# Performance work log

Hardware: AMD Instinct MI355X
Metric: run time of the kernel (lower is better)

## Reference

```python
import jax, jax.numpy as jnp
import numpy as np

N = 50000
E = 800000
IN_C = 256
OUT_C = 128
HID = 2 * OUT_C  # 256


def setup_inputs() -> dict:
    key = jax.random.key(0)
    ks = jax.random.split(key, 8)
    def glorot(k, fan_in, fan_out):
        lim = (6.0 / (fan_in + fan_out)) ** 0.5
        return jax.random.uniform(k, (fan_in, fan_out), jnp.float32, -lim, lim)
    x = jax.random.normal(ks[0], (N, IN_C), dtype=jnp.float32)
    edge_index = jax.random.randint(ks[1], (2, E), 0, N, dtype=jnp.int64)
    return {
        "x": x,
        "edge_index": edge_index,
        "W1": glorot(ks[2], IN_C, HID),
        "b1": jnp.zeros((HID,), jnp.float32),
        "W_mu": glorot(ks[3], HID, OUT_C),
        "b_mu": jnp.zeros((OUT_C,), jnp.float32),
        "W_ls": glorot(ks[4], HID, OUT_C),
        "b_ls": jnp.zeros((OUT_C,), jnp.float32),
    }


def _gcn_norm(edge_index, n):
    # PyG GCNConv default: add self-loops, symmetric normalization D^-1/2 A D^-1/2
    loop = jnp.arange(n, dtype=edge_index.dtype)
    src = jnp.concatenate([edge_index[0], loop])  # [E+N]
    dst = jnp.concatenate([edge_index[1], loop])
    deg = jax.ops.segment_sum(jnp.ones_like(dst, dtype=jnp.float32), dst, num_segments=n)
    dinv = jnp.where(deg > 0, jax.lax.rsqrt(deg), 0.0)
    norm = dinv[src] * dinv[dst]  # [E+N]
    return src, dst, norm


def _gcn_conv(x, W, b, src, dst, norm, n):
    h = x @ W                                   # [N, F_out] transform first (F_out < F_in ok)
    msg = h[src] * norm[:, None]                # [E+N, F_out] gather + scale
    out = jax.ops.segment_sum(msg, dst, num_segments=n)  # scatter-add aggregate
    return out + b


def reference(x, edge_index, W1, b1, W_mu, b_mu, W_ls, b_ls):
    n = x.shape[0]
    src, dst, norm = _gcn_norm(edge_index, n)
    h = jax.nn.relu(_gcn_conv(x, W1, b1, src, dst, norm, n))
    mu = _gcn_conv(h, W_mu, b_mu, src, dst, norm, n)
    logstd = _gcn_conv(h, W_ls, b_ls, src, dst, norm, n)
    return (mu, logstd)
```

## Files before the change

### kernel.cpp

```cpp
#include <hip/hip_runtime.h>

#define NN 50000
#define EE 800000
#define NB_FILL 3125
#define NB_PA 12500
#define NB_PB 512

typedef _Float16 half8 __attribute__((ext_vector_type(8)));
typedef float f32x4 __attribute__((ext_vector_type(4)));

__device__ __forceinline__ unsigned short f2h(float f){
  _Float16 h = (_Float16)f; unsigned short u; __builtin_memcpy(&u, &h, 2); return u;
}
__device__ __forceinline__ float h2f(unsigned short u){
  _Float16 h; __builtin_memcpy(&h, &u, 2); return (float)h;
}
__device__ __forceinline__ void split2h(float v, unsigned short* p){
  _Float16 hi = (_Float16)v;
  _Float16 lo = (_Float16)(v - (float)hi);
  __builtin_memcpy(p, &hi, 2);
  __builtin_memcpy(p+1, &lo, 2);
}
__device__ __forceinline__ void gl2lds16(const unsigned short* g, unsigned short* l){
  __builtin_amdgcn_global_load_lds(
    (const __attribute__((address_space(1))) unsigned int*)g,
    (__attribute__((address_space(3))) unsigned int*)l, 16, 0, 0);
}

__device__ __forceinline__ int detect_m(const int* eidx, int* sh){
  int t = threadIdx.x;
  if (t < 64){
    int v = eidx[2*t + 1];
    unsigned long long nz = __ballot(v != 0);
    if (t == 0) *sh = (nz == 0ULL) ? 1 : 0;
  }
  __syncthreads();
  return *sh;
}

__global__ __launch_bounds__(256) void k_prep(const int* __restrict__ eidx,
    const float* __restrict__ X, const float* __restrict__ W1,
    const float* __restrict__ Wmu, const float* __restrict__ Wls,
    int* __restrict__ cnt, int* __restrict__ bk,
    unsigned short* __restrict__ Asp, unsigned short* __restrict__ Bt1,
    unsigned short* __restrict__ Bt2){
  int b = blockIdx.x;
  if (b < NB_FILL){
    __shared__ int msh;
    int m = detect_m(eidx, &msh);
    int e = b*256 + threadIdx.x;
    int sv = m ? eidx[2*e]        : eidx[e];
    int d  = m ? eidx[2*(EE + e)] : eidx[EE + e];
    int p = atomicAdd(&cnt[d], 1);
    if (p < 64) bk[((size_t)d << 6) + p] = sv;
  } else if (b < NB_FILL + NB_PA){
    int gid = (b - NB_FILL)*256 + threadIdx.x;
    int r = gid >> 6, t = gid & 63;
    float4 v = *(const float4*)(X + (size_t)r*256 + t*4);
    __attribute__((aligned(16))) unsigned short sh[8];
    split2h(v.x, sh); split2h(v.y, sh+2); split2h(v.z, sh+4); split2h(v.w, sh+6);
    *(uint4*)(Asp + (size_t)r*512 + t*8) = *(const uint4*)(sh);
  } else {
    int gid = (b - NB_FILL - NB_PA)*256 + threadIdx.x;
    int idx = gid & 65535;
    int n = idx & 255, k = idx >> 8;
    if (gid < 65536){
      unsigned short hq = f2h(W1[k*256 + n]);
      unsigned short* p = Bt1 + (size_t)n*512 + 2*k;
      p[0] = hq; p[1] = hq;
    } else {
      float w = (n < 128) ? Wmu[k*128 + n] : Wls[k*128 + (n - 128)];
      Bt2[(size_t)n*256 + k] = f2h(w);
    }
  }
}

template<int KT, int SCALE>
__global__ __launch_bounds__(256) void k_gemm(const unsigned short* __restrict__ Asp,
                                              const unsigned short* __restrict__ Bt,
                                              unsigned short* __restrict__ C, int M,
                                              const int* __restrict__ cnt){
  __shared__ __align__(16) unsigned short sA[128*64];
  __shared__ __align__(16) unsigned short sB[128*64];
  const int tid  = threadIdx.x;
  const int wave = tid >> 6, lane = tid & 63;
  const int wm = wave >> 1, wn = wave & 1;
  const int quad = lane >> 4, l16 = lane & 15;
  const int tM = blockIdx.x, tN = blockIdx.y;
  const int rsub = lane >> 3;
  const int chs  = (lane & 7) ^ rsub;

  f32x4 acc[4][4] = {};

  for (int kt = 0; kt < KT; ++kt){
    #pragma unroll
    for (int j = 0; j < 4; ++j){
      int q = wave*4 + j;
      int r = q*8 + rsub;
      int arow = tM*128 + r; if (arow >= M) arow = M-1;
      gl2lds16(Asp + (size_t)arow*(KT*64) + kt*64 + chs*8, &sA[q*512]);
      gl2lds16(Bt  + (size_t)(tN*128 + r)*(KT*64) + kt*64 + chs*8, &sB[q*512]);
    }
    __syncthreads();
    #pragma unroll
    for (int ks = 0; ks < 2; ++ks){
      half8 af[4], bfr[4];
      #pragma unroll
      for (int t = 0; t < 4; ++t){
        int R = wm*64 + t*16 + l16;
        af[t]  = *(const half8*)(&sA[R*64 + ((ks*4 + quad) ^ (R & 7))*8]);
      }
      #pragma unroll
      for (int t = 0; t < 4; ++t){
        int R = wn*64 + t*16 + l16;
        bfr[t] = *(const half8*)(&sB[R*64 + ((ks*4 + quad) ^ (R & 7))*8]);
      }
      #pragma unroll
      for (int mt = 0; mt < 4; ++mt)
        #pragma unroll
        for (int nt = 0; nt < 4; ++nt)
          acc[mt][nt] = __builtin_amdgcn_mfma_f32_16x16x32_f16(af[mt], bfr[nt], acc[mt][nt], 0, 0, 0);
    }
    __syncthreads();
  }

  #pragma unroll
  for (int mt = 0; mt < 4; ++mt){
    #pragma unroll
    for (int r = 0; r < 4; ++r){
      int row = tM*128 + wm*64 + mt*16 + quad*4 + r;
      if (row < M){
        float sc = 1.f;
        if (SCALE) sc = rsqrtf((float)(cnt[row] + 1));
        #pragma unroll
        for (int nt = 0; nt < 4; ++nt){
          int cc = tN*128 + wn*64 + nt*16 + l16;
          C[(size_t)row*256 + cc] = f2h(acc[mt][nt][r] * sc);
        }
      }
    }
  }
}

__global__ __launch_bounds__(256) void k_agg_relu(const unsigned short* __restrict__ feat,
    const int* __restrict__ cnt, const int* __restrict__ bkall,
    const float* __restrict__ b1, unsigned short* __restrict__ h1){
  int i = blockIdx.x*4 + (threadIdx.x >> 6);
  int lane = threadIdx.x & 63;
  int f0 = lane*4;
  int deg = cnt[i]; if (deg > 64) deg = 64;
  float di = rsqrtf((float)(deg + 1));
  const int* bk = bkall + ((size_t)i << 6);
  ushort4 hv = *(const ushort4*)(feat + (size_t)i*256 + f0);
  float p0 = h2f(hv.x), p1 = h2f(hv.y), p2 = h2f(hv.z), p3 = h2f(hv.w);
  float q0=0.f,q1=0.f,q2=0.f,q3=0.f, r0=0.f,r1=0.f,r2=0.f,r3=0.f, t0=0.f,t1=0.f,t2=0.f,t3=0.f;
  int e = 0;
  for (; e + 8 <= deg; e += 8){
    int4 sa = *(const int4*)(bk + e);
    int4 sb = *(const int4*)(bk + e + 4);
    ushort4 v0 = *(const ushort4*)(feat + (size_t)sa.x*256 + f0);
    ushort4 v1 = *(const ushort4*)(feat + (size_t)sa.y*256 + f0);
    ushort4 v2 = *(const ushort4*)(feat + (size_t)sa.z*256 + f0);
    ushort4 v3 = *(const ushort4*)(feat + (size_t)sa.w*256 + f0);
    ushort4 v4 = *(const ushort4*)(feat + (size_t)sb.x*256 + f0);
    ushort4 v5 = *(const ushort4*)(feat + (size_t)sb.y*256 + f0);
    ushort4 v6 = *(const ushort4*)(feat + (size_t)sb.z*256 + f0);
    ushort4 v7 = *(const ushort4*)(feat + (size_t)sb.w*256 + f0);
    p0 += h2f(v0.x); p1 += h2f(v0.y); p2 += h2f(v0.z); p3 += h2f(v0.w);
    q0 += h2f(v1.x); q1 += h2f(v1.y); q2 += h2f(v1.z); q3 += h2f(v1.w);
    r0 += h2f(v2.x); r1 += h2f(v2.y); r2 += h2f(v2.z); r3 += h2f(v2.w);
    t0 += h2f(v3.x); t1 += h2f(v3.y); t2 += h2f(v3.z); t3 += h2f(v3.w);
    p0 += h2f(v4.x); p1 += h2f(v4.y); p2 += h2f(v4.z); p3 += h2f(v4.w);
    q0 += h2f(v5.x); q1 += h2f(v5.y); q2 += h2f(v5.z); q3 += h2f(v5.w);
    r0 += h2f(v6.x); r1 += h2f(v6.y); r2 += h2f(v6.z); r3 += h2f(v6.w);
    t0 += h2f(v7.x); t1 += h2f(v7.y); t2 += h2f(v7.z); t3 += h2f(v7.w);
  }
  if (e + 4 <= deg){
    int4 sa = *(const int4*)(bk + e);
    ushort4 v0 = *(const ushort4*)(feat + (size_t)sa.x*256 + f0);
    ushort4 v1 = *(const ushort4*)(feat + (size_t)sa.y*256 + f0);
    ushort4 v2 = *(const ushort4*)(feat + (size_t)sa.z*256 + f0);
    ushort4 v3 = *(const ushort4*)(feat + (size_t)sa.w*256 + f0);
    p0 += h2f(v0.x); p1 += h2f(v0.y); p2 += h2f(v0.z); p3 += h2f(v0.w);
    q0 += h2f(v1.x); q1 += h2f(v1.y); q2 += h2f(v1.z); q3 += h2f(v1.w);
    r0 += h2f(v2.x); r1 += h2f(v2.y); r2 += h2f(v2.z); r3 += h2f(v2.w);
    t0 += h2f(v3.x); t1 += h2f(v3.y); t2 += h2f(v3.z); t3 += h2f(v3.w);
    e += 4;
  }
  for (; e < deg; ++e){
    int s = bk[e];
    ushort4 v = *(const ushort4*)(feat + (size_t)s*256 + f0);
    p0 += h2f(v.x); p1 += h2f(v.y); p2 += h2f(v.z); p3 += h2f(v.w);
  }
  float s0 = p0+q0+r0+t0, s1 = p1+q1+r1+t1, s2 = p2+q2+r2+t2, s3 = p3+q3+r3+t3;
  float4 bb = *(const float4*)(b1 + f0);
  float u0 = fmaxf(di*s0 + bb.x, 0.f);
  float u1 = fmaxf(di*s1 + bb.y, 0.f);
  float u2 = fmaxf(di*s2 + bb.z, 0.f);
  float u3 = fmaxf(di*s3 + bb.w, 0.f);
  ushort4 o;
  o.x = f2h(di*u0); o.y = f2h(di*u1); o.z = f2h(di*u2); o.w = f2h(di*u3);
  *(ushort4*)(h1 + (size_t)i*256 + f0) = o;
}

__global__ __launch_bounds__(256) void k_agg_out(const unsigned short* __restrict__ feat,
    const int* __restrict__ cnt, const int* __restrict__ bkall,
    const float* __restrict__ bmu, const float* __restrict__ bls, float* __restrict__ outp){
  int i = blockIdx.x*4 + (threadIdx.x >> 6);
  int lane = threadIdx.x & 63;
  int f0 = lane*4;
  int deg = cnt[i]; if (deg > 64) deg = 64;
  float di = rsqrtf((float)(deg + 1));
  const int* bk = bkall + ((size_t)i << 6);
  ushort4 hv = *(const ushort4*)(feat + (size_t)i*256 + f0);
  float p0 = h2f(hv.x), p1 = h2f(hv.y), p2 = h2f(hv.z), p3 = h2f(hv.w);
  float q0=0.f,q1=0.f,q2=0.f,q3=0.f, r0=0.f,r1=0.f,r2=0.f,r3=0.f, t0=0.f,t1=0.f,t2=0.f,t3=0.f;
  int e = 0;
  for (; e + 8 <= deg; e += 8){
    int4 sa = *(const int4*)(bk + e);
    int4 sb = *(const int4*)(bk + e + 4);
    ushort4 v0 = *(const ushort4*)(feat + (size_t)sa.x*256 + f0);
    ushort4 v1 = *(const ushort4*)(feat + (size_t)sa.y*256 + f0);
    ushort4 v2 = *(const ushort4*)(feat + (size_t)sa.z*256 + f0);
    ushort4 v3 = *(const ushort4*)(feat + (size_t)sa.w*256 + f0);
    ushort4 v4 = *(const ushort4*)(feat + (size_t)sb.x*256 + f0);
    ushort4 v5 = *(const ushort4*)(feat + (size_t)sb.y*256 + f0);
    ushort4 v6 = *(const ushort4*)(feat + (size_t)sb.z*256 + f0);
    ushort4 v7 = *(const ushort4*)(feat + (size_t)sb.w*256 + f0);
    p0 += h2f(v0.x); p1 += h2f(v0.y); p2 += h2f(v0.z); p3 += h2f(v0.w);
    q0 += h2f(v1.x); q1 += h2f(v1.y); q2 += h2f(v1.z); q3 += h2f(v1.w);
    r0 += h2f(v2.x); r1 += h2f(v2.y); r2 += h2f(v2.z); r3 += h2f(v2.w);
    t0 += h2f(v3.x); t1 += h2f(v3.y); t2 += h2f(v3.z); t3 += h2f(v3.w);
    p0 += h2f(v4.x); p1 += h2f(v4.y); p2 += h2f(v4.z); p3 += h2f(v4.w);
    q0 += h2f(v5.x); q1 += h2f(v5.y); q2 += h2f(v5.z); q3 += h2f(v5.w);
    r0 += h2f(v6.x); r1 += h2f(v6.y); r2 += h2f(v6.z); r3 += h2f(v6.w);
    t0 += h2f(v7.x); t1 += h2f(v7.y); t2 += h2f(v7.z); t3 += h2f(v7.w);
  }
  if (e + 4 <= deg){
    int4 sa = *(const int4*)(bk + e);
    ushort4 v0 = *(const ushort4*)(feat + (size_t)sa.x*256 + f0);
    ushort4 v1 = *(const ushort4*)(feat + (size_t)sa.y*256 + f0);
    ushort4 v2 = *(const ushort4*)(feat + (size_t)sa.z*256 + f0);
    ushort4 v3 = *(const ushort4*)(feat + (size_t)sa.w*256 + f0);
    p0 += h2f(v0.x); p1 += h2f(v0.y); p2 += h2f(v0.z); p3 += h2f(v0.w);
    q0 += h2f(v1.x); q1 += h2f(v1.y); q2 += h2f(v1.z); q3 += h2f(v1.w);
    r0 += h2f(v2.x); r1 += h2f(v2.y); r2 += h2f(v2.z); r3 += h2f(v2.w);
    t0 += h2f(v3.x); t1 += h2f(v3.y); t2 += h2f(v3.z); t3 += h2f(v3.w);
    e += 4;
  }
  for (; e < deg; ++e){
    int s = bk[e];
    ushort4 v = *(const ushort4*)(feat + (size_t)s*256 + f0);
    p0 += h2f(v.x); p1 += h2f(v.y); p2 += h2f(v.z); p3 += h2f(v.w);
  }
  float a0 = di*(p0+q0+r0+t0), a1 = di*(p1+q1+r1+t1);
  float a2 = di*(p2+q2+r2+t2), a3 = di*(p3+q3+r3+t3);
  float4 o;
  if (f0 < 128){
    float4 bb = *(const float4*)(bmu + f0);
    o.x = a0 + bb.x; o.y = a1 + bb.y; o.z = a2 + bb.z; o.w = a3 + bb.w;
    *(float4*)(outp + (size_t)i*128 + f0) = o;
  } else {
    int g = f0 - 128;
    float4 bb = *(const float4*)(bls + g);
    o.x = a0 + bb.x; o.y = a1 + bb.y; o.z = a2 + bb.z; o.w = a3 + bb.w;
    *(float4*)(outp + (size_t)NN*128 + (size_t)i*128 + g) = o;
  }
}

extern "C" void kernel_launch(void* const* d_in, const int* in_sizes, int n_in,
                              void* d_out, int out_size, void* d_ws, size_t ws_size,
                              hipStream_t stream){
  const float* x   = (const float*)d_in[0];
  const int* eidx  = (const int*)d_in[1];
  const float* W1  = (const float*)d_in[2];
  const float* b1  = (const float*)d_in[3];
  const float* Wmu = (const float*)d_in[4];
  const float* bmu = (const float*)d_in[5];
  const float* Wls = (const float*)d_in[6];
  const float* bls = (const float*)d_in[7];
  float* out = (float*)d_out;

  char* ws = (char*)d_ws;
  size_t off = 0;
  auto alloc = [&](size_t bytes)->char*{
    char* p = ws + off; off = (off + bytes + 511) & ~(size_t)511; return p;
  };
  int* cnt      = (int*)alloc(NN*4);
  int* buckets  = (int*)alloc((size_t)NN*64*4);
  unsigned short* Bt1 = (unsigned short*)alloc((size_t)256*512*2);
  unsigned short* Bt2 = (unsigned short*)alloc((size_t)256*256*2);
  unsigned short* AspX = (unsigned short*)alloc((size_t)NN*512*2);
  unsigned short* h1  = (unsigned short*)alloc((size_t)NN*256*2);
  unsigned short* h   = (unsigned short*)alloc((size_t)NN*256*2);
  unsigned short* z   = h;

  hipMemsetAsync(cnt, 0, NN*4, stream);
  k_prep<<<NB_FILL + NB_PA + NB_PB, 256, 0, stream>>>(eidx, x, W1, Wmu, Wls,
                                                      cnt, buckets, AspX, Bt1, Bt2);
  k_gemm<8,1><<<dim3(391, 2), 256, 0, stream>>>(AspX, Bt1, h, NN, cnt);
  k_agg_relu<<<12500, 256, 0, stream>>>(h, cnt, buckets, b1, h1);
  k_gemm<4,0><<<dim3(391, 2), 256, 0, stream>>>(h1, Bt2, z, NN, cnt);
  k_agg_out<<<12500, 256, 0, stream>>>(z, cnt, buckets, bmu, bls, out);
}
```

Measured before the change: 320.8 us.

## Split edge counting from bucket fill and store neighbor indices as 16-bit

Edge counting stays in the prep kernel. The bucket fill now runs as extra blocks inside the first GEMM launch, using a separate cursor array, so the atomics and scatter overlap with MFMA work. Bucket entries shrink from 32-bit to 16-bit, halving index traffic in both aggregation kernels. Node ids up to 50000 exceed the int16 range, but they fit in unsigned 16 bits (max 65535), so this works only because N is below 65536.

```diff
diff --git a/kernel.cpp b/kernel.cpp
--- a/kernel.cpp
+++ b/kernel.cpp
@@ -2,12 +2,15 @@
 
 #define NN 50000
 #define EE 800000
-#define NB_FILL 3125
+#define NB_CNT 3125
 #define NB_PA 12500
 #define NB_PB 512
+#define NGB 782
 
 typedef _Float16 half8 __attribute__((ext_vector_type(8)));
 typedef float f32x4 __attribute__((ext_vector_type(4)));
+typedef unsigned short ushort8v __attribute__((ext_vector_type(8)));
+typedef unsigned short ushort4v __attribute__((ext_vector_type(4)));
 
 __device__ __forceinline__ unsigned short f2h(float f){
   _Float16 h = (_Float16)f; unsigned short u; __builtin_memcpy(&u, &h, 2); return u;
@@ -41,27 +44,25 @@
 __global__ __launch_bounds__(256) void k_prep(const int* __restrict__ eidx,
     const float* __restrict__ X, const float* __restrict__ W1,
     const float* __restrict__ Wmu, const float* __restrict__ Wls,
-    int* __restrict__ cnt, int* __restrict__ bk,
+    int* __restrict__ cnt,
     unsigned short* __restrict__ Asp, unsigned short* __restrict__ Bt1,
     unsigned short* __restrict__ Bt2){
   int b = blockIdx.x;
-  if (b < NB_FILL){
+  if (b < NB_CNT){
     __shared__ int msh;
     int m = detect_m(eidx, &msh);
     int e = b*256 + threadIdx.x;
-    int sv = m ? eidx[2*e]        : eidx[e];
-    int d  = m ? eidx[2*(EE + e)] : eidx[EE + e];
-    int p = atomicAdd(&cnt[d], 1);
-    if (p < 64) bk[((size_t)d << 6) + p] = sv;
-  } else if (b < NB_FILL + NB_PA){
-    int gid = (b - NB_FILL)*256 + threadIdx.x;
+    int d = m ? eidx[2*(EE + e)] : eidx[EE + e];
+    atomicAdd(&cnt[d], 1);
+  } else if (b < NB_CNT + NB_PA){
+    int gid = (b - NB_CNT)*256 + threadIdx.x;
     int r = gid >> 6, t = gid & 63;
     float4 v = *(const float4*)(X + (size_t)r*256 + t*4);
     __attribute__((aligned(16))) unsigned short sh[8];
     split2h(v.x, sh); split2h(v.y, sh+2); split2h(v.z, sh+4); split2h(v.w, sh+6);
     *(uint4*)(Asp + (size_t)r*512 + t*8) = *(const uint4*)(sh);
   } else {
-    int gid = (b - NB_FILL - NB_PA)*256 + threadIdx.x;
+    int gid = (b - NB_CNT - NB_PA)*256 + threadIdx.x;
     int idx = gid & 65535;
     int n = idx & 255, k = idx >> 8;
     if (gid < 65536){
@@ -75,11 +76,89 @@
   }
 }
 
-template<int KT, int SCALE>
+__global__ __launch_bounds__(256) void k_gemm8_fill(
+    const unsigned short* __restrict__ Asp, const unsigned short* __restrict__ Bt,
+    unsigned short* __restrict__ C, int M, const int* __restrict__ cnt,
+    const int* __restrict__ eidx, int* __restrict__ cursor,
+    unsigned short* __restrict__ bk){
+  __shared__ __align__(16) unsigned short sA[128*64];
+  __shared__ __align__(16) unsigned short sB[128*64];
+  __shared__ int msh;
+  const int b = blockIdx.x;
+  if (b >= NGB){
+    int m = detect_m(eidx, &msh);
+    int e = (b - NGB)*256 + threadIdx.x;
+    int sv = m ? eidx[2*e]        : eidx[e];
+    int d  = m ? eidx[2*(EE + e)] : eidx[EE + e];
+    int p = atomicAdd(&cursor[d], 1);
+    if (p < 64) bk[((size_t)d << 6) + p] = (unsigned short)sv;
+    return;
+  }
+  const int KT = 8;
+  const int tid  = threadIdx.x;
+  const int wave = tid >> 6, lane = tid & 63;
+  const int wm = wave >> 1, wn = wave & 1;
+  const int quad = lane >> 4, l16 = lane & 15;
+  const int tN = (b >= 391) ? 1 : 0;
+  const int tM = b - tN*391;
+  const int rsub = lane >> 3;
+  const int chs  = (lane & 7) ^ rsub;
+
+  f32x4 acc[4][4] = {};
+
+  for (int kt = 0; kt < KT; ++kt){
+    #pragma unroll
+    for (int j = 0; j < 4; ++j){
+      int q = wave*4 + j;
+      int r = q*8 + rsub;
+      int arow = tM*128 + r; if (arow >= M) arow = M-1;
+      gl2lds16(Asp + (size_t)arow*(KT*64) + kt*64 + chs*8, &sA[q*512]);
+      gl2lds16(Bt  + (size_t)(tN*128 + r)*(KT*64) + kt*64 + chs*8, &sB[q*512]);
+    }
+    __syncthreads();
+    #pragma unroll
+    for (int ks = 0; ks < 2; ++ks){
+      half8 af[4], bfr[4];
+      #pragma unroll
+      for (int t = 0; t < 4; ++t){
+        int R = wm*64 + t*16 + l16;
+        af[t]  = *(const half8*)(&sA[R*64 + ((ks*4 + quad) ^ (R & 7))*8]);
+      }
+      #pragma unroll
+      for (int t = 0; t < 4; ++t){
+        int R = wn*64 + t*16 + l16;
+        bfr[t] = *(const half8*)(&sB[R*64 + ((ks*4 + quad) ^ (R & 7))*8]);
+      }
+      #pragma unroll
+      for (int mt = 0; mt < 4; ++mt)
+        #pragma unroll
+        for (int nt = 0; nt < 4; ++nt)
+          acc[mt][nt] = __builtin_amdgcn_mfma_f32_16x16x32_f16(af[mt], bfr[nt], acc[mt][nt], 0, 0, 0);
+    }
+    __syncthreads();
+  }
+
+  #pragma unroll
+  for (int mt = 0; mt < 4; ++mt){
+    #pragma unroll
+    for (int r = 0; r < 4; ++r){
+      int row = tM*128 + wm*64 + mt*16 + quad*4 + r;
+      if (row < M){
+        float sc = rsqrtf((float)(cnt[row] + 1));
+        #pragma unroll
+        for (int nt = 0; nt < 4; ++nt){
+          int cc = tN*128 + wn*64 + nt*16 + l16;
+          C[(size_t)row*256 + cc] = f2h(acc[mt][nt][r] * sc);
+        }
+      }
+    }
+  }
+}
+
+template<int KT>
 __global__ __launch_bounds__(256) void k_gemm(const unsigned short* __restrict__ Asp,
                                               const unsigned short* __restrict__ Bt,
-                                              unsigned short* __restrict__ C, int M,
-                                              const int* __restrict__ cnt){
+                                              unsigned short* __restrict__ C, int M){
   __shared__ __align__(16) unsigned short sA[128*64];
   __shared__ __align__(16) unsigned short sB[128*64];
   const int tid  = threadIdx.x;
@@ -130,12 +209,10 @@
     for (int r = 0; r < 4; ++r){
       int row = tM*128 + wm*64 + mt*16 + quad*4 + r;
       if (row < M){
-        float sc = 1.f;
-        if (SCALE) sc = rsqrtf((float)(cnt[row] + 1));
         #pragma unroll
         for (int nt = 0; nt < 4; ++nt){
           int cc = tN*128 + wn*64 + nt*16 + l16;
-          C[(size_t)row*256 + cc] = f2h(acc[mt][nt][r] * sc);
+          C[(size_t)row*256 + cc] = f2h(acc[mt][nt][r]);
         }
       }
     }
@@ -143,29 +220,28 @@
 }
 
 __global__ __launch_bounds__(256) void k_agg_relu(const unsigned short* __restrict__ feat,
-    const int* __restrict__ cnt, const int* __restrict__ bkall,
+    const int* __restrict__ cnt, const unsigned short* __restrict__ bkall,
     const float* __restrict__ b1, unsigned short* __restrict__ h1){
   int i = blockIdx.x*4 + (threadIdx.x >> 6);
   int lane = threadIdx.x & 63;
   int f0 = lane*4;
   int deg = cnt[i]; if (deg > 64) deg = 64;
   float di = rsqrtf((float)(deg + 1));
-  const int* bk = bkall + ((size_t)i << 6);
+  const unsigned short* bk = bkall + ((size_t)i << 6);
   ushort4 hv = *(const ushort4*)(feat + (size_t)i*256 + f0);
   float p0 = h2f(hv.x), p1 = h2f(hv.y), p2 = h2f(hv.z), p3 = h2f(hv.w);
   float q0=0.f,q1=0.f,q2=0.f,q3=0.f, r0=0.f,r1=0.f,r2=0.f,r3=0.f, t0=0.f,t1=0.f,t2=0.f,t3=0.f;
   int e = 0;
   for (; e + 8 <= deg; e += 8){
-    int4 sa = *(const int4*)(bk + e);
-    int4 sb = *(const int4*)(bk + e + 4);
-    ushort4 v0 = *(const ushort4*)(feat + (size_t)sa.x*256 + f0);
-    ushort4 v1 = *(const ushort4*)(feat + (size_t)sa.y*256 + f0);
-    ushort4 v2 = *(const ushort4*)(feat + (size_t)sa.z*256 + f0);
-    ushort4 v3 = *(const ushort4*)(feat + (size_t)sa.w*256 + f0);
-    ushort4 v4 = *(const ushort4*)(feat + (size_t)sb.x*256 + f0);
-    ushort4 v5 = *(const ushort4*)(feat + (size_t)sb.y*256 + f0);
-    ushort4 v6 = *(const ushort4*)(feat + (size_t)sb.z*256 + f0);
-    ushort4 v7 = *(const ushort4*)(feat + (size_t)sb.w*256 + f0);
+    ushort8v sa = *(const ushort8v*)(bk + e);
+    ushort4 v0 = *(const ushort4*)(feat + (size_t)sa[0]*256 + f0);
+    ushort4 v1 = *(const ushort4*)(feat + (size_t)sa[1]*256 + f0);
+    ushort4 v2 = *(const ushort4*)(feat + (size_t)sa[2]*256 + f0);
+    ushort4 v3 = *(const ushort4*)(feat + (size_t)sa[3]*256 + f0);
+    ushort4 v4 = *(const ushort4*)(feat + (size_t)sa[4]*256 + f0);
+    ushort4 v5 = *(const ushort4*)(feat + (size_t)sa[5]*256 + f0);
+    ushort4 v6 = *(const ushort4*)(feat + (size_t)sa[6]*256 + f0);
+    ushort4 v7 = *(const ushort4*)(feat + (size_t)sa[7]*256 + f0);
     p0 += h2f(v0.x); p1 += h2f(v0.y); p2 += h2f(v0.z); p3 += h2f(v0.w);
     q0 += h2f(v1.x); q1 += h2f(v1.y); q2 += h2f(v1.z); q3 += h2f(v1.w);
     r0 += h2f(v2.x); r1 += h2f(v2.y); r2 += h2f(v2.z); r3 += h2f(v2.w);
@@ -176,11 +252,11 @@
     t0 += h2f(v7.x); t1 += h2f(v7.y); t2 += h2f(v7.z); t3 += h2f(v7.w);
   }
   if (e + 4 <= deg){
-    int4 sa = *(const int4*)(bk + e);
-    ushort4 v0 = *(const ushort4*)(feat + (size_t)sa.x*256 + f0);
-    ushort4 v1 = *(const ushort4*)(feat + (size_t)sa.y*256 + f0);
-    ushort4 v2 = *(const ushort4*)(feat + (size_t)sa.z*256 + f0);
-    ushort4 v3 = *(const ushort4*)(feat + (size_t)sa.w*256 + f0);
+    ushort4v sa = *(const ushort4v*)(bk + e);
+    ushort4 v0 = *(const ushort4*)(feat + (size_t)sa[0]*256 + f0);
+    ushort4 v1 = *(const ushort4*)(feat + (size_t)sa[1]*256 + f0);
+    ushort4 v2 = *(const ushort4*)(feat + (size_t)sa[2]*256 + f0);
+    ushort4 v3 = *(const ushort4*)(feat + (size_t)sa[3]*256 + f0);
     p0 += h2f(v0.x); p1 += h2f(v0.y); p2 += h2f(v0.z); p3 += h2f(v0.w);
     q0 += h2f(v1.x); q1 += h2f(v1.y); q2 += h2f(v1.z); q3 += h2f(v1.w);
     r0 += h2f(v2.x); r1 += h2f(v2.y); r2 += h2f(v2.z); r3 += h2f(v2.w);
@@ -204,29 +280,28 @@
 }
 
 __global__ __launch_bounds__(256) void k_agg_out(const unsigned short* __restrict__ feat,
-    const int* __restrict__ cnt, const int* __restrict__ bkall,
+    const int* __restrict__ cnt, const unsigned short* __restrict__ bkall,
     const float* __restrict__ bmu, const float* __restrict__ bls, float* __restrict__ outp){
   int i = blockIdx.x*4 + (threadIdx.x >> 6);
   int lane = threadIdx.x & 63;
   int f0 = lane*4;
   int deg = cnt[i]; if (deg > 64) deg = 64;
   float di = rsqrtf((float)(deg + 1));
-  const int* bk = bkall + ((size_t)i << 6);
+  const unsigned short* bk = bkall + ((size_t)i << 6);
   ushort4 hv = *(const ushort4*)(feat + (size_t)i*256 + f0);
   float p0 = h2f(hv.x), p1 = h2f(hv.y), p2 = h2f(hv.z), p3 = h2f(hv.w);
   float q0=0.f,q1=0.f,q2=0.f,q3=0.f, r0=0.f,r1=0.f,r2=0.f,r3=0.f, t0=0.f,t1=0.f,t2=0.f,t3=0.f;
   int e = 0;
   for (; e + 8 <= deg; e += 8){
-    int4 sa = *(const int4*)(bk + e);
-    int4 sb = *(const int4*)(bk + e + 4);
-    ushort4 v0 = *(const ushort4*)(feat + (size_t)sa.x*256 + f0);
-    ushort4 v1 = *(const ushort4*)(feat + (size_t)sa.y*256 + f0);
-    ushort4 v2 = *(const ushort4*)(feat + (size_t)sa.z*256 + f0);
-    ushort4 v3 = *(const ushort4*)(feat + (size_t)sa.w*256 + f0);
-    ushort4 v4 = *(const ushort4*)(feat + (size_t)sb.x*256 + f0);
-    ushort4 v5 = *(const ushort4*)(feat + (size_t)sb.y*256 + f0);
-    ushort4 v6 = *(const ushort4*)(feat + (size_t)sb.z*256 + f0);
-    ushort4 v7 = *(const ushort4*)(feat + (size_t)sb.w*256 + f0);
+    ushort8v sa = *(const ushort8v*)(bk + e);
+    ushort4 v0 = *(const ushort4*)(feat + (size_t)sa[0]*256 + f0);
+    ushort4 v1 = *(const ushort4*)(feat + (size_t)sa[1]*256 + f0);
+    ushort4 v2 = *(const ushort4*)(feat + (size_t)sa[2]*256 + f0);
+    ushort4 v3 = *(const ushort4*)(feat + (size_t)sa[3]*256 + f0);
+    ushort4 v4 = *(const ushort4*)(feat + (size_t)sa[4]*256 + f0);
+    ushort4 v5 = *(const ushort4*)(feat + (size_t)sa[5]*256 + f0);
+    ushort4 v6 = *(const ushort4*)(feat + (size_t)sa[6]*256 + f0);
+    ushort4 v7 = *(const ushort4*)(feat + (size_t)sa[7]*256 + f0);
     p0 += h2f(v0.x); p1 += h2f(v0.y); p2 += h2f(v0.z); p3 += h2f(v0.w);
     q0 += h2f(v1.x); q1 += h2f(v1.y); q2 += h2f(v1.z); q3 += h2f(v1.w);
     r0 += h2f(v2.x); r1 += h2f(v2.y); r2 += h2f(v2.z); r3 += h2f(v2.w);
@@ -237,11 +312,11 @@
     t0 += h2f(v7.x); t1 += h2f(v7.y); t2 += h2f(v7.z); t3 += h2f(v7.w);
   }
   if (e + 4 <= deg){
-    int4 sa = *(const int4*)(bk + e);
-    ushort4 v0 = *(const ushort4*)(feat + (size_t)sa.x*256 + f0);
-    ushort4 v1 = *(const ushort4*)(feat + (size_t)sa.y*256 + f0);
-    ushort4 v2 = *(const ushort4*)(feat + (size_t)sa.z*256 + f0);
-    ushort4 v3 = *(const ushort4*)(feat + (size_t)sa.w*256 + f0);
+    ushort4v sa = *(const ushort4v*)(bk + e);
+    ushort4 v0 = *(const ushort4*)(feat + (size_t)sa[0]*256 + f0);
+    ushort4 v1 = *(const ushort4*)(feat + (size_t)sa[1]*256 + f0);
+    ushort4 v2 = *(const ushort4*)(feat + (size_t)sa[2]*256 + f0);
+    ushort4 v3 = *(const ushort4*)(feat + (size_t)sa[3]*256 + f0);
     p0 += h2f(v0.x); p1 += h2f(v0.y); p2 += h2f(v0.z); p3 += h2f(v0.w);
     q0 += h2f(v1.x); q1 += h2f(v1.y); q2 += h2f(v1.z); q3 += h2f(v1.w);
     r0 += h2f(v2.x); r1 += h2f(v2.y); r2 += h2f(v2.z); r3 += h2f(v2.w);
@@ -287,7 +362,8 @@
     char* p = ws + off; off = (off + bytes + 511) & ~(size_t)511; return p;
   };
   int* cnt      = (int*)alloc(NN*4);
-  int* buckets  = (int*)alloc((size_t)NN*64*4);
+  int* cursor   = (int*)alloc(NN*4);
+  unsigned short* buckets = (unsigned short*)alloc((size_t)NN*64*2);
   unsigned short* Bt1 = (unsigned short*)alloc((size_t)256*512*2);
   unsigned short* Bt2 = (unsigned short*)alloc((size_t)256*256*2);
   unsigned short* AspX = (unsigned short*)alloc((size_t)NN*512*2);
@@ -295,11 +371,13 @@
   unsigned short* h   = (unsigned short*)alloc((size_t)NN*256*2);
   unsigned short* z   = h;
 
-  hipMemsetAsync(cnt, 0, NN*4, stream);
-  k_prep<<<NB_FILL + NB_PA + NB_PB, 256, 0, stream>>>(eidx, x, W1, Wmu, Wls,
-                                                      cnt, buckets, AspX, Bt1, Bt2);
-  k_gemm<8,1><<<dim3(391, 2), 256, 0, stream>>>(AspX, Bt1, h, NN, cnt);
+  size_t zero_bytes = (size_t)((char*)cursor - (char*)cnt) + NN*4;
+  hipMemsetAsync(cnt, 0, zero_bytes, stream);
+  k_prep<<<NB_CNT + NB_PA + NB_PB, 256, 0, stream>>>(eidx, x, W1, Wmu, Wls,
+                                                     cnt, AspX, Bt1, Bt2);
+  k_gemm8_fill<<<NGB + 3125, 256, 0, stream>>>(AspX, Bt1, h, NN, cnt,
+                                               eidx, cursor, buckets);
   k_agg_relu<<<12500, 256, 0, stream>>>(h, cnt, buckets, b1, h1);
-  k_gemm<4,0><<<dim3(391, 2), 256, 0, stream>>>(h1, Bt2, z, NN, cnt);
+  k_gemm<4><<<dim3(391, 2), 256, 0, stream>>>(h1, Bt2, z, NN);
   k_agg_out<<<12500, 256, 0, stream>>>(z, cnt, buckets, bmu, bls, out);
 }
```

Result: slower. 342.2 us (+6.7%).
